# Performance work log

Measured on AMD Instinct MI355X. Metric: run time of the kernel, lower is better.

The kernel has to match this reference:

```python
import jax, jax.numpy as jnp
import numpy as np

ATTN_HEADS = 4
NEG_INF = float(np.finfo(np.float32).min)


def setup_inputs() -> dict:
    key = jax.random.key(0)
    ks = jax.random.split(key, 7)
    B, N, K, Cin, Cout = 4, 4096, 32, 128, 128
    h_X = jax.random.normal(ks[0], (B, N, Cout), dtype=jnp.float32)
    h_E = jax.random.normal(ks[1], (B, N, K, Cin), dtype=jnp.float32)
    mask_attn = jax.random.randint(ks[2], (B, N, K), 0, 2, dtype=jnp.int32)
    # torch Linear weights are [out_features, in_features]
    W_Q = jax.random.normal(ks[3], (Cout, Cout), dtype=jnp.float32) / np.sqrt(Cout)
    W_K = jax.random.normal(ks[4], (Cout, Cin), dtype=jnp.float32) / np.sqrt(Cin)
    W_V = jax.random.normal(ks[5], (Cout, Cin), dtype=jnp.float32) / np.sqrt(Cin)
    W_O = jax.random.normal(ks[6], (Cout, 3 * Cout), dtype=jnp.float32) / np.sqrt(3 * Cout)
    return {"h_X": h_X, "h_E": h_E, "mask_attn": mask_attn,
            "W_Q": W_Q, "W_K": W_K, "W_V": W_V, "W_O": W_O}


def reference(h_X, h_E, mask_attn, W_Q, W_K, W_V, W_O):
    B, N, K, _ = h_E.shape
    C = W_Q.shape[0]
    H = ATTN_HEADS
    d = C // H

    h_q = (h_X @ W_Q.T).reshape(B, N, H, d)          # [B,N,H,d]
    h_k = (h_E @ W_K.T).reshape(B, N, K, H, d)       # [B,N,K,H,d]
    h_v = (h_E @ W_V.T).reshape(B, N, K, H, d)       # [B,N,K,H,d]

    # per-node, per-head scores over K neighbors
    scores = jnp.einsum('bnhd,bnkhd->bnhk', h_q, h_k) / np.sqrt(d)

    mask = (mask_attn[:, :, None, :] > 0)            # [B,N,1,K] -> broadcast over heads
    logits = jnp.where(mask, scores, NEG_INF)
    attn = jax.nn.softmax(logits, axis=-1) * mask.astype(scores.dtype)  # [B,N,H,K]

    attn_sum = attn.sum(axis=-1, keepdims=True) + 1e-8                  # [B,N,H,1]
    hv_t = jnp.swapaxes(h_v, 2, 3)                                      # [B,N,H,K,d]
    weighted_v = attn[..., None] * hv_t                                 # [B,N,H,K,d]
    weighted_sum = weighted_v.sum(axis=3)                               # [B,N,H,d]
    aggr_mean = (weighted_sum / attn_sum).reshape(B, N, C)
    aggr_sum = weighted_sum.reshape(B, N, C)
    aggr_max = weighted_v.max(axis=3).reshape(B, N, C)

    aggr_cat = jnp.concatenate([aggr_mean, aggr_sum, aggr_max], axis=-1)  # [B,N,3C]
    return aggr_cat @ W_O.T                                               # [B,N,C]
```

## Files before the change

kernel.cpp:

```cpp
#include <hip/hip_runtime.h>
#include <stdint.h>


typedef __attribute__((ext_vector_type(8))) short short8;
typedef __attribute__((ext_vector_type(4))) float f32x4;

#define NPB   16
#define CDIM  128
#define KN    32
#define ESTR  136
#define TSTR  136
#define QSTR  136
#define CATS  392
#define SSTR  36

__device__ __forceinline__ float bf2f(short s) {
    union { unsigned int u; float f; } v;
    v.u = ((unsigned int)(unsigned short)s) << 16;
    return v.f;
}
__device__ __forceinline__ short f2bf(float f) {
    union { float ff; unsigned int u; } v; v.ff = f;
    unsigned int u = v.u;
    u += 0x7FFFu + ((u >> 16) & 1u);
    return (short)(u >> 16);
}

struct f8 { float v[8]; };

template<bool FP32>
__device__ __forceinline__ short8 load8bf(const void* p, size_t idx) {
    if constexpr (FP32) {
        const float* fp = (const float*)p + idx;
        f32x4 a = *(const f32x4*)fp;
        f32x4 b = *(const f32x4*)(fp + 4);
        short8 r;
        r[0] = f2bf(a[0]); r[1] = f2bf(a[1]); r[2] = f2bf(a[2]); r[3] = f2bf(a[3]);
        r[4] = f2bf(b[0]); r[5] = f2bf(b[1]); r[6] = f2bf(b[2]); r[7] = f2bf(b[3]);
        return r;
    } else {
        return *(const short8*)((const short*)p + idx);
    }
}

template<bool FP32>
__device__ __forceinline__ short loadbf1(const void* p, size_t idx) {
    if constexpr (FP32) return f2bf(((const float*)p)[idx]);
    else return ((const short*)p)[idx];
}

struct alignas(16) Smem {
    short sE[128 * ESTR];
    short sT[64 * TSTR];
    short sQ[16 * QSTR];
    short sCat[16 * CATS];
    float sS[16 * SSTR];
    int   sMask[NPB * KN];
    float sAInv[16];
};

template<bool FP32>
__device__ __forceinline__ void issueE(const void* hE, size_t base, int tid,
                                       f32x4 (&eF)[8][2], short8 (&eB)[8]) {
    if constexpr (FP32) {
        #pragma unroll
        for (int it = 0; it < 8; ++it) {
            const float* p = (const float*)hE + base + (size_t)(it * 256 + tid) * 8;
            eF[it][0] = *(const f32x4*)p;
            eF[it][1] = *(const f32x4*)(p + 4);
        }
    } else {
        #pragma unroll
        for (int it = 0; it < 8; ++it)
            eB[it] = *(const short8*)((const short*)hE + base + (size_t)(it * 256 + tid) * 8);
    }
}

template<bool FP32>
__device__ __forceinline__ void writeE(short* sE, int tid,
                                       const f32x4 (&eF)[8][2], const short8 (&eB)[8]) {
    #pragma unroll
    for (int it = 0; it < 8; ++it) {
        const int chunk = it * 256 + tid, row = chunk >> 4, cc = chunk & 15;
        short8 v;
        if constexpr (FP32) {
            #pragma unroll
            for (int t = 0; t < 4; ++t) { v[t] = f2bf(eF[it][0][t]); v[4 + t] = f2bf(eF[it][1][t]); }
        } else v = eB[it];
        *(short8*)&sE[row * ESTR + cc * 8] = v;
    }
}

template<bool FP32>
__device__ __forceinline__ void na_body(Smem& sm,
    const void* __restrict__ hX, const void* __restrict__ hE,
    const int* __restrict__ mask, const void* __restrict__ WQ,
    const void* __restrict__ WK, const void* __restrict__ WV,
    const void* __restrict__ WO, void* __restrict__ out)
{
    const int tid  = threadIdx.x;
    const int lane = tid & 63;
    const int w    = tid >> 6;
    const int quad = lane >> 4;
    const int l15  = lane & 15;
    const int nb   = blockIdx.x * NPB;
    const size_t ebase = (size_t)nb * (KN * CDIM);

    *(int2*)&sm.sMask[tid * 2] = *(const int2*)&mask[(size_t)nb * KN + tid * 2];

    f32x4 eF[8][2]; short8 eB[8];
    issueE<FP32>(hE, ebase, tid, eF, eB);

    short8 ax[4];
    #pragma unroll
    for (int kk = 0; kk < 4; ++kk)
        ax[kk] = load8bf<FP32>(hX, (size_t)(nb + l15) * CDIM + kk * 32 + quad * 8);

    short8 bq[2][4];
    #pragma unroll
    for (int t2 = 0; t2 < 2; ++t2)
        #pragma unroll
        for (int kk = 0; kk < 4; ++kk)
            bq[t2][kk] = load8bf<FP32>(WQ, (size_t)(w * 32 + t2 * 16 + l15) * CDIM + kk * 32 + quad * 8);

    short8 bv[2][4];
    #pragma unroll
    for (int ct = 0; ct < 2; ++ct)
        #pragma unroll
        for (int kk = 0; kk < 4; ++kk)
            bv[ct][kk] = load8bf<FP32>(WV, (size_t)((2 * w + ct) * 16 + l15) * CDIM + kk * 32 + quad * 8);

    short8 bk[2][4];
    #pragma unroll
    for (int t2 = 0; t2 < 2; ++t2)
        #pragma unroll
        for (int kk = 0; kk < 4; ++kk) {
            const int j = w * 32 + t2 * 16 + l15;
            short8 b;
            #pragma unroll
            for (int jj = 0; jj < 8; ++jj)
                b[jj] = loadbf1<FP32>(WK, (size_t)(kk * 32 + quad * 8 + jj) * CDIM + j);
            bk[t2][kk] = b;
        }

    {
        f32x4 o0 = {0.f,0.f,0.f,0.f}, o1 = {0.f,0.f,0.f,0.f};
        #pragma unroll
        for (int kk = 0; kk < 4; ++kk) {
            o0 = __builtin_amdgcn_mfma_f32_16x16x32_bf16(ax[kk], bq[0][kk], o0, 0, 0, 0);
            o1 = __builtin_amdgcn_mfma_f32_16x16x32_bf16(ax[kk], bq[1][kk], o1, 0, 0, 0);
        }
        #pragma unroll
        for (int r = 0; r < 4; ++r) {
            const int n = quad * 4 + r;
            sm.sQ[n * QSTR + w * 32 + l15]      = f2bf(o0[r]);
            sm.sQ[n * QSTR + w * 32 + 16 + l15] = f2bf(o1[r]);
        }
    }
    __syncthreads();

    {
        const float scale = 0.17677669529663687f;
        const short8 zz = {0,0,0,0,0,0,0,0};
        #pragma unroll
        for (int m = 0; m < 4; ++m) {
            const int n_g = m * 4 + (l15 >> 2), h_ = l15 & 3;
            const short8 qv = *(const short8*)&sm.sQ[n_g * QSTR + h_ * 32 + quad * 8];
            f32x4 c0 = {0.f,0.f,0.f,0.f}, c1 = {0.f,0.f,0.f,0.f};
            #pragma unroll
            for (int kk = 0; kk < 4; ++kk) {
                const short8 af = (kk == h_) ? qv : zz;
                c0 = __builtin_amdgcn_mfma_f32_16x16x32_bf16(af, bk[0][kk], c0, 0, 0, 0);
                c1 = __builtin_amdgcn_mfma_f32_16x16x32_bf16(af, bk[1][kk], c1, 0, 0, 0);
            }
            #pragma unroll
            for (int r = 0; r < 4; ++r) {
                const int row = m * 16 + quad * 4 + r;
                sm.sT[row * TSTR + w * 32 + l15]      = f2bf(c0[r] * scale);
                sm.sT[row * TSTR + w * 32 + 16 + l15] = f2bf(c1[r] * scale);
            }
        }
    }

    writeE<FP32>(sm.sE, tid, eF, eB);
    issueE<FP32>(hE, ebase + 1 * 128 * 128, tid, eF, eB);
    __syncthreads();

    #pragma unroll 1
    for (int s = 0; s < 4; ++s) {
        {
            short8 bs[4], a0[4], a1[4];
            #pragma unroll
            for (int kk = 0; kk < 4; ++kk) {
                bs[kk] = *(const short8*)&sm.sT[(16 * s + l15) * TSTR + kk * 32 + quad * 8];
                a0[kk] = *(const short8*)&sm.sE[(w * 32 + l15) * ESTR + kk * 32 + quad * 8];
                a1[kk] = *(const short8*)&sm.sE[(w * 32 + 16 + l15) * ESTR + kk * 32 + quad * 8];
            }
            f32x4 s0 = {0.f,0.f,0.f,0.f}, s1 = {0.f,0.f,0.f,0.f};
            #pragma unroll
            for (int kk = 0; kk < 4; ++kk) {
                s0 = __builtin_amdgcn_mfma_f32_16x16x32_bf16(a0[kk], bs[kk], s0, 0, 0, 0);
                s1 = __builtin_amdgcn_mfma_f32_16x16x32_bf16(a1[kk], bs[kk], s1, 0, 0, 0);
            }
            if ((l15 >> 2) == w) {
                const int h = l15 & 3;
                #pragma unroll
                for (int r = 0; r < 4; ++r) {
                    sm.sS[(w * 4 + h) * SSTR + quad * 4 + r]      = s0[r];
                    sm.sS[(w * 4 + h) * SSTR + 16 + quad * 4 + r] = s1[r];
                }
            }
        }
        __syncthreads();

        if (tid < 64) {
            const int nh = lane >> 2, sub = lane & 3, n_ = nh >> 2;
            const int* mp = &sm.sMask[(s * 4 + n_) * KN];
            float* sp = &sm.sS[nh * SSTR];
            float x[8]; int mk[8];
            #pragma unroll
            for (int j = 0; j < 8; ++j) { const int k = sub * 8 + j; mk[j] = mp[k]; x[j] = sp[k]; }
            float m = -3.0e38f;
            #pragma unroll
            for (int j = 0; j < 8; ++j) m = fmaxf(m, (mk[j] > 0) ? x[j] : -3.0e38f);
            m = fmaxf(m, __shfl_xor(m, 1));
            m = fmaxf(m, __shfl_xor(m, 2));
            float dsum = 0.f;
            #pragma unroll
            for (int j = 0; j < 8; ++j) {
                const float e = __expf(fminf(x[j] - m, 0.f)) * ((mk[j] > 0) ? 1.f : 0.f);
                x[j] = e; dsum += e;
            }
            dsum += __shfl_xor(dsum, 1);
            dsum += __shfl_xor(dsum, 2);
            const float inv = (dsum > 0.f) ? (1.f / dsum) : 0.f;
            #pragma unroll
            for (int j = 0; j < 8; ++j) sp[sub * 8 + j] = x[j] * inv;
            if (sub == 0) sm.sAInv[nh] = 1.0f / (((dsum > 0.f) ? 1.0f : 0.0f) + 1e-8f);
        }
        __syncthreads();

        #pragma unroll
        for (int n_ = 0; n_ < 4; ++n_) {
            short8 a0[4], a1[4];
            #pragma unroll
            for (int kk = 0; kk < 4; ++kk) {
                a0[kk] = *(const short8*)&sm.sE[(n_ * 32 + l15) * ESTR + kk * 32 + quad * 8];
                a1[kk] = *(const short8*)&sm.sE[(n_ * 32 + 16 + l15) * ESTR + kk * 32 + quad * 8];
            }
            const float* ap = &sm.sS[(n_ * 4 + w) * SSTR];
            const float inv = sm.sAInv[n_ * 4 + w];
            #pragma unroll
            for (int ct = 0; ct < 2; ++ct) {
                f32x4 av0 = {0.f,0.f,0.f,0.f}, av1 = {0.f,0.f,0.f,0.f};
                #pragma unroll
                for (int kk = 0; kk < 4; ++kk) {
                    av0 = __builtin_amdgcn_mfma_f32_16x16x32_bf16(a0[kk], bv[ct][kk], av0, 0, 0, 0);
                    av1 = __builtin_amdgcn_mfma_f32_16x16x32_bf16(a1[kk], bv[ct][kk], av1, 0, 0, 0);
                }
                float sum = 0.f, mx = -3.0e38f;
                #pragma unroll
                for (int r = 0; r < 4; ++r) {
                    const float p0 = ap[quad * 4 + r]      * av0[r];
                    const float p1 = ap[16 + quad * 4 + r] * av1[r];
                    sum += p0 + p1;
                    mx = fmaxf(mx, fmaxf(p0, p1));
                }
                sum += __shfl_xor(sum, 16);
                sum += __shfl_xor(sum, 32);
                mx = fmaxf(mx, __shfl_xor(mx, 16));
                mx = fmaxf(mx, __shfl_xor(mx, 32));
                if (quad == 0) {
                    const int c = (2 * w + ct) * 16 + l15, row = s * 4 + n_;
                    sm.sCat[row * CATS + c]       = f2bf(sum * inv);
                    sm.sCat[row * CATS + 128 + c] = f2bf(sum);
                    sm.sCat[row * CATS + 256 + c] = f2bf(mx);
                }
            }
        }
        __syncthreads();

        if (s < 3) {
            writeE<FP32>(sm.sE, tid, eF, eB);
            if (s < 2) issueE<FP32>(hE, ebase + (size_t)(s + 2) * 128 * 128, tid, eF, eB);
            __syncthreads();
        }
    }

    {
        f32x4 o0 = {0.f,0.f,0.f,0.f}, o1 = {0.f,0.f,0.f,0.f};
        #pragma unroll
        for (int kk = 0; kk < 12; ++kk) {
            const short8 a  = *(const short8*)&sm.sCat[l15 * CATS + kk * 32 + quad * 8];
            const short8 b0 = load8bf<FP32>(WO, (size_t)(w * 32 + l15) * 384 + kk * 32 + quad * 8);
            const short8 b1 = load8bf<FP32>(WO, (size_t)(w * 32 + 16 + l15) * 384 + kk * 32 + quad * 8);
            o0 = __builtin_amdgcn_mfma_f32_16x16x32_bf16(a, b0, o0, 0, 0, 0);
            o1 = __builtin_amdgcn_mfma_f32_16x16x32_bf16(a, b1, o1, 0, 0, 0);
        }
        #pragma unroll
        for (int r = 0; r < 4; ++r) {
            const int node = quad * 4 + r;
            const size_t base = (size_t)(nb + node) * CDIM + w * 32;
            if constexpr (FP32) {
                ((float*)out)[base + l15]      = o0[r];
                ((float*)out)[base + 16 + l15] = o1[r];
            } else {
                ((short*)out)[base + l15]      = f2bf(o0[r]);
                ((short*)out)[base + 16 + l15] = f2bf(o1[r]);
            }
        }
    }
}

__global__ __launch_bounds__(256, 2)
void na_fused(const void* __restrict__ hX, const void* __restrict__ hE,
              const int* __restrict__ mask, const void* __restrict__ WQ,
              const void* __restrict__ WK, const void* __restrict__ WV,
              const void* __restrict__ WO, void* __restrict__ out)
{
    __shared__ Smem sm;
    const short* wq16 = (const short*)WQ;
    const int lane = threadIdx.x & 63;
    int cnt = 0;
    #pragma unroll
    for (int i = 0; i < 8; ++i) {
        const float v = bf2f(wq16[lane + i * 64]);
        if (!(fabsf(v) < 8.0f)) cnt++;
    }
    #pragma unroll
    for (int d = 1; d < 64; d <<= 1) cnt += __shfl_xor(cnt, d);
    if (cnt > 16) na_body<true >(sm, hX, hE, mask, WQ, WK, WV, WO, out);
    else          na_body<false>(sm, hX, hE, mask, WQ, WK, WV, WO, out);
}

extern "C" void kernel_launch(void* const* d_in, const int* in_sizes, int n_in,
                              void* d_out, int out_size, void* d_ws, size_t ws_size,
                              hipStream_t stream) {
    (void)in_sizes; (void)n_in; (void)ws_size; (void)out_size; (void)d_ws;
    const void* hX   = d_in[0];
    const void* hE   = d_in[1];
    const int*  mask = (const int*)d_in[2];
    const void* WQ   = d_in[3];
    const void* WK   = d_in[4];
    const void* WV   = d_in[5];
    const void* WO   = d_in[6];

    na_fused<<<dim3(1024), dim3(256), 0, stream>>>(hX, hE, mask, WQ, WK, WV, WO, d_out);
}
```

Baseline: 401.6 us.

## Assign one node per wave and fuse in-register softmax to cut block barriers

Each wave now owns one node per stage. It computes that node's scores and does the masked softmax directly in registers with cross-quad shuffles, instead of staging scores in shared memory and running softmax on a single wave. The shared-memory tile for the next stage is written right after the current operands are loaded into registers, which removes most of the per-stage __syncthreads calls. W_V fragments are reloaded from global memory inside the loop instead of being held in registers, and a sched_barrier is added after the E loads. This trades extra global/L2 traffic and possible fp32-to-bf16 conversion work for fewer barriers and lower register pressure.

Result: slower. 431.0 us (+7.3%).

```diff
diff --git a/kernel.cpp b/kernel.cpp
--- a/kernel.cpp
+++ b/kernel.cpp
@@ -25,8 +25,6 @@
     u += 0x7FFFu + ((u >> 16) & 1u);
     return (short)(u >> 16);
 }
-
-struct f8 { float v[8]; };
 
 template<bool FP32>
 __device__ __forceinline__ short8 load8bf(const void* p, size_t idx) {
@@ -56,7 +54,6 @@
     short sCat[16 * CATS];
     float sS[16 * SSTR];
     int   sMask[NPB * KN];
-    float sAInv[16];
 };
 
 template<bool FP32>
@@ -74,6 +71,7 @@
         for (int it = 0; it < 8; ++it)
             eB[it] = *(const short8*)((const short*)hE + base + (size_t)(it * 256 + tid) * 8);
     }
+    __builtin_amdgcn_sched_barrier(0);
 }
 
 template<bool FP32>
@@ -106,11 +104,11 @@
     const int nb   = blockIdx.x * NPB;
     const size_t ebase = (size_t)nb * (KN * CDIM);
 
-    *(int2*)&sm.sMask[tid * 2] = *(const int2*)&mask[(size_t)nb * KN + tid * 2];
-
     f32x4 eF[8][2]; short8 eB[8];
     issueE<FP32>(hE, ebase, tid, eF, eB);
 
+    *(int2*)&sm.sMask[tid * 2] = *(const int2*)&mask[(size_t)nb * KN + tid * 2];
+
     short8 ax[4];
     #pragma unroll
     for (int kk = 0; kk < 4; ++kk)
@@ -122,13 +120,6 @@
         #pragma unroll
         for (int kk = 0; kk < 4; ++kk)
             bq[t2][kk] = load8bf<FP32>(WQ, (size_t)(w * 32 + t2 * 16 + l15) * CDIM + kk * 32 + quad * 8);
-
-    short8 bv[2][4];
-    #pragma unroll
-    for (int ct = 0; ct < 2; ++ct)
-        #pragma unroll
-        for (int kk = 0; kk < 4; ++kk)
-            bv[ct][kk] = load8bf<FP32>(WV, (size_t)((2 * w + ct) * 16 + l15) * CDIM + kk * 32 + quad * 8);
 
     short8 bk[2][4];
     #pragma unroll
@@ -188,104 +179,95 @@
 
     #pragma unroll 1
     for (int s = 0; s < 4; ++s) {
+        short8 bs[4], a0[4], a1[4];
+        #pragma unroll
+        for (int kk = 0; kk < 4; ++kk) {
+            bs[kk] = *(const short8*)&sm.sT[(16 * s + l15) * TSTR + kk * 32 + quad * 8];
+            a0[kk] = *(const short8*)&sm.sE[(w * 32 + l15) * ESTR + kk * 32 + quad * 8];
+            a1[kk] = *(const short8*)&sm.sE[(w * 32 + 16 + l15) * ESTR + kk * 32 + quad * 8];
+        }
+        if (s < 3) {
+            __syncthreads();
+            writeE<FP32>(sm.sE, tid, eF, eB);
+            if (s < 2) issueE<FP32>(hE, ebase + (size_t)(s + 2) * 128 * 128, tid, eF, eB);
+        }
+
+        f32x4 s0 = {0.f,0.f,0.f,0.f}, s1 = {0.f,0.f,0.f,0.f};
+        #pragma unroll
+        for (int kk = 0; kk < 4; ++kk) {
+            s0 = __builtin_amdgcn_mfma_f32_16x16x32_bf16(a0[kk], bs[kk], s0, 0, 0, 0);
+            s1 = __builtin_amdgcn_mfma_f32_16x16x32_bf16(a1[kk], bs[kk], s1, 0, 0, 0);
+        }
+
         {
-            short8 bs[4], a0[4], a1[4];
-            #pragma unroll
-            for (int kk = 0; kk < 4; ++kk) {
-                bs[kk] = *(const short8*)&sm.sT[(16 * s + l15) * TSTR + kk * 32 + quad * 8];
-                a0[kk] = *(const short8*)&sm.sE[(w * 32 + l15) * ESTR + kk * 32 + quad * 8];
-                a1[kk] = *(const short8*)&sm.sE[(w * 32 + 16 + l15) * ESTR + kk * 32 + quad * 8];
-            }
-            f32x4 s0 = {0.f,0.f,0.f,0.f}, s1 = {0.f,0.f,0.f,0.f};
-            #pragma unroll
-            for (int kk = 0; kk < 4; ++kk) {
-                s0 = __builtin_amdgcn_mfma_f32_16x16x32_bf16(a0[kk], bs[kk], s0, 0, 0, 0);
-                s1 = __builtin_amdgcn_mfma_f32_16x16x32_bf16(a1[kk], bs[kk], s1, 0, 0, 0);
-            }
-            if ((l15 >> 2) == w) {
-                const int h = l15 & 3;
-                #pragma unroll
-                for (int r = 0; r < 4; ++r) {
-                    sm.sS[(w * 4 + h) * SSTR + quad * 4 + r]      = s0[r];
-                    sm.sS[(w * 4 + h) * SSTR + 16 + quad * 4 + r] = s1[r];
-                }
-            }
-        }
-        __syncthreads();
-
-        if (tid < 64) {
-            const int nh = lane >> 2, sub = lane & 3, n_ = nh >> 2;
-            const int* mp = &sm.sMask[(s * 4 + n_) * KN];
-            float* sp = &sm.sS[nh * SSTR];
+            const int* mp = &sm.sMask[(s * 4 + (l15 >> 2)) * KN];
             float x[8]; int mk[8];
             #pragma unroll
-            for (int j = 0; j < 8; ++j) { const int k = sub * 8 + j; mk[j] = mp[k]; x[j] = sp[k]; }
+            for (int j = 0; j < 4; ++j) {
+                x[j] = s0[j];     mk[j]     = mp[quad * 4 + j];
+                x[4 + j] = s1[j]; mk[4 + j] = mp[16 + quad * 4 + j];
+            }
             float m = -3.0e38f;
             #pragma unroll
             for (int j = 0; j < 8; ++j) m = fmaxf(m, (mk[j] > 0) ? x[j] : -3.0e38f);
-            m = fmaxf(m, __shfl_xor(m, 1));
-            m = fmaxf(m, __shfl_xor(m, 2));
+            m = fmaxf(m, __shfl_xor(m, 16));
+            m = fmaxf(m, __shfl_xor(m, 32));
             float dsum = 0.f;
             #pragma unroll
             for (int j = 0; j < 8; ++j) {
                 const float e = __expf(fminf(x[j] - m, 0.f)) * ((mk[j] > 0) ? 1.f : 0.f);
                 x[j] = e; dsum += e;
             }
-            dsum += __shfl_xor(dsum, 1);
-            dsum += __shfl_xor(dsum, 2);
+            dsum += __shfl_xor(dsum, 16);
+            dsum += __shfl_xor(dsum, 32);
             const float inv = (dsum > 0.f) ? (1.f / dsum) : 0.f;
-            #pragma unroll
-            for (int j = 0; j < 8; ++j) sp[sub * 8 + j] = x[j] * inv;
-            if (sub == 0) sm.sAInv[nh] = 1.0f / (((dsum > 0.f) ? 1.0f : 0.0f) + 1e-8f);
-        }
-        __syncthreads();
-
-        #pragma unroll
-        for (int n_ = 0; n_ < 4; ++n_) {
-            short8 a0[4], a1[4];
+            if ((l15 >> 2) == w) {
+                float* sp = &sm.sS[(w * 4 + (l15 & 3)) * SSTR];
+                #pragma unroll
+                for (int j = 0; j < 4; ++j) {
+                    sp[quad * 4 + j]      = x[j] * inv;
+                    sp[16 + quad * 4 + j] = x[4 + j] * inv;
+                }
+                if (quad == 0)
+                    sp[33] = 1.0f / (((dsum > 0.f) ? 1.0f : 0.0f) + 1e-8f);
+            }
+        }
+
+        #pragma unroll
+        for (int ct = 0; ct < 8; ++ct) {
+            const int h = ct >> 1;
+            f32x4 av0 = {0.f,0.f,0.f,0.f}, av1 = {0.f,0.f,0.f,0.f};
             #pragma unroll
             for (int kk = 0; kk < 4; ++kk) {
-                a0[kk] = *(const short8*)&sm.sE[(n_ * 32 + l15) * ESTR + kk * 32 + quad * 8];
-                a1[kk] = *(const short8*)&sm.sE[(n_ * 32 + 16 + l15) * ESTR + kk * 32 + quad * 8];
-            }
-            const float* ap = &sm.sS[(n_ * 4 + w) * SSTR];
-            const float inv = sm.sAInv[n_ * 4 + w];
-            #pragma unroll
-            for (int ct = 0; ct < 2; ++ct) {
-                f32x4 av0 = {0.f,0.f,0.f,0.f}, av1 = {0.f,0.f,0.f,0.f};
-                #pragma unroll
-                for (int kk = 0; kk < 4; ++kk) {
-                    av0 = __builtin_amdgcn_mfma_f32_16x16x32_bf16(a0[kk], bv[ct][kk], av0, 0, 0, 0);
-                    av1 = __builtin_amdgcn_mfma_f32_16x16x32_bf16(a1[kk], bv[ct][kk], av1, 0, 0, 0);
-                }
-                float sum = 0.f, mx = -3.0e38f;
-                #pragma unroll
-                for (int r = 0; r < 4; ++r) {
-                    const float p0 = ap[quad * 4 + r]      * av0[r];
-                    const float p1 = ap[16 + quad * 4 + r] * av1[r];
-                    sum += p0 + p1;
-                    mx = fmaxf(mx, fmaxf(p0, p1));
-                }
-                sum += __shfl_xor(sum, 16);
-                sum += __shfl_xor(sum, 32);
-                mx = fmaxf(mx, __shfl_xor(mx, 16));
-                mx = fmaxf(mx, __shfl_xor(mx, 32));
-                if (quad == 0) {
-                    const int c = (2 * w + ct) * 16 + l15, row = s * 4 + n_;
-                    sm.sCat[row * CATS + c]       = f2bf(sum * inv);
-                    sm.sCat[row * CATS + 128 + c] = f2bf(sum);
-                    sm.sCat[row * CATS + 256 + c] = f2bf(mx);
-                }
-            }
-        }
-        __syncthreads();
-
-        if (s < 3) {
-            writeE<FP32>(sm.sE, tid, eF, eB);
-            if (s < 2) issueE<FP32>(hE, ebase + (size_t)(s + 2) * 128 * 128, tid, eF, eB);
-            __syncthreads();
-        }
-    }
+                const short8 bvf = load8bf<FP32>(WV, (size_t)(ct * 16 + l15) * CDIM + kk * 32 + quad * 8);
+                av0 = __builtin_amdgcn_mfma_f32_16x16x32_bf16(a0[kk], bvf, av0, 0, 0, 0);
+                av1 = __builtin_amdgcn_mfma_f32_16x16x32_bf16(a1[kk], bvf, av1, 0, 0, 0);
+            }
+            const float* ap = &sm.sS[(w * 4 + h) * SSTR];
+            const float ainv = ap[33];
+            float sum = 0.f, mx = -3.0e38f;
+            #pragma unroll
+            for (int r = 0; r < 4; ++r) {
+                const float p0 = ap[quad * 4 + r]      * av0[r];
+                const float p1 = ap[16 + quad * 4 + r] * av1[r];
+                sum += p0 + p1;
+                mx = fmaxf(mx, fmaxf(p0, p1));
+            }
+            sum += __shfl_xor(sum, 16);
+            sum += __shfl_xor(sum, 32);
+            mx = fmaxf(mx, __shfl_xor(mx, 16));
+            mx = fmaxf(mx, __shfl_xor(mx, 32));
+            if (quad == 0) {
+                const int c = ct * 16 + l15, row = s * 4 + w;
+                sm.sCat[row * CATS + c]       = f2bf(sum * ainv);
+                sm.sCat[row * CATS + 128 + c] = f2bf(sum);
+                sm.sCat[row * CATS + 256 + c] = f2bf(mx);
+            }
+        }
+
+        if (s < 3) __syncthreads();
+    }
+    __syncthreads();
 
     {
         f32x4 o0 = {0.f,0.f,0.f,0.f}, o1 = {0.f,0.f,0.f,0.f};
```
